# Kernel tuning notes

Hardware: AMD Instinct MI355X
Metric: run time of the kernel (lower is better)

## Reference

```python
import jax, jax.numpy as jnp
import numpy as np

# Dimensions (see shape_source): k=4 -> hk=cobj_size=2
K_LEVEL = 4
HK = K_LEVEL // 2            # conv kernel/stride, == cobj_size
BS = 16                      # MBS*ncobj groups
NUM_TOP = 512
BAG = 50                     # bag size B (orig_fea.shape[1])
D = 512                      # feature dim
H = 512                      # relation-unit hidden dim


def setup_inputs() -> dict:
    key = jax.random.key(0)
    ks = jax.random.split(key, 7)
    orig_fea = jax.random.normal(ks[0], (BS * 2 * HK, BAG, D), jnp.float32)
    ind0 = jax.random.randint(ks[1], (BS, NUM_TOP, HK), 0, BAG, jnp.int32)
    ind1 = jax.random.randint(ks[2], (BS, NUM_TOP, HK), 0, BAG, jnp.int32)
    W0 = jax.random.normal(ks[3], (D, H), jnp.float32) * 0.05
    W1 = jax.random.normal(ks[4], (D, H), jnp.float32) * 0.05
    b = jax.random.normal(ks[5], (H,), jnp.float32) * 0.05
    v = jax.random.normal(ks[6], (H,), jnp.float32) * 0.05
    return {"orig_fea": orig_fea, "ind0": ind0, "ind1": ind1,
            "W0": W0, "W1": W1, "b": b, "v": v}


def reference(orig_fea, ind0, ind1, W0, W1, b, v):
    bs = ind0.shape[0]
    bag = orig_fea.shape[1]
    cobj = ind0.shape[-1]                 # == k//2 == conv kernel hk
    d = orig_fea.shape[-1]

    # create_ids: offset by bag * position so ids index into the flattened half
    offs = (bag * jnp.arange(cobj)).astype(ind0.dtype)
    ids0 = (ind0 + offs).reshape(bs, -1)  # [bs, S], S = num_top*cobj
    ids1 = (ind1 + offs).reshape(bs, -1)

    # rsolo_fea: [bs, 2, X, D] with X = bag*cobj
    fea = orig_fea.reshape(bs, 2, -1, d)

    # relation unit over ALL X*X candidate pairs (dedupe+gather-back in the
    # original is pure memoization; compute-then-gather is the same math)
    h0 = jnp.einsum('bxd,dh->bxh', fea[:, 0], W0)   # [bs, X, H]
    h1 = jnp.einsum('byd,dh->byh', fea[:, 1], W1)   # [bs, X, H]
    hid = jax.nn.relu(h0[:, :, None, :] + h1[:, None, :, :] + b)  # [bs, X, X, H]
    full = jnp.einsum('bxyh,h->bxy', hid, v)        # [bs, X, X]

    # gather rows by ids0, cols by ids1 (per group)
    scores = jax.vmap(lambda f, i0, i1: f[i0][:, i1])(full, ids0, ids1)  # [bs, S, S]

    # Conv2D(1, kernel=hk, stride=hk, ones kernel, zero bias) == block sum-pool
    S = scores.shape[1]
    hk = cobj
    pooled = scores.reshape(bs, S // hk, hk, S // hk, hk).sum(axis=(2, 4))  # [bs, nt, nt]
    out_scores = pooled.reshape(bs, -1, 1)          # [bs, nt*nt, 1]

    nt0, nt1 = ind0.shape[1], ind1.shape[1]
    gi, gj = jnp.meshgrid(jnp.arange(nt0, dtype=jnp.int32),
                          jnp.arange(nt1, dtype=jnp.int32), indexing='ij')
    pairs = jnp.broadcast_to(jnp.stack([gi, gj], axis=-1)[None],
                             (bs, nt0, nt1, 2)).reshape(bs, nt0 * nt1, 2)
    return out_scores, pairs
```

## Files before the change

kernel.cpp:

```cpp
#include <hip/hip_runtime.h>

#define XDIM  100
#define DDIM  512
#define HDIM  512
#define NT    512
#define WS_WT2   0
#define WS_FEA16 1048576
#define WS_V16   4325376
#define WS_H16   4326400
#define WS_FP    7603200

typedef _Float16 h16x8 __attribute__((ext_vector_type(8)));
typedef _Float16 h2    __attribute__((ext_vector_type(2)));
typedef float floatx4  __attribute__((ext_vector_type(4)));

union H8U { h16x8 v; h2 p[4]; unsigned u[4]; };

__global__ void __launch_bounds__(256) prep_k(const float* __restrict__ W0,
                                              const float* __restrict__ W1,
                                              const float* __restrict__ fea,
                                              const float* __restrict__ v,
                                              _Float16* __restrict__ Wt2,
                                              _Float16* __restrict__ fea16,
                                              _Float16* __restrict__ v16) {
    int blk = blockIdx.x;
    int t = threadIdx.x;
    if (blk < 2048) {
        int o  = blk * 256 + t;
        int w  = o >> 18;
        int kb = (o >> 14) & 15;
        int c  = (o >> 5) & 511;
        int qj = o & 31;
        int d  = kb * 32 + qj;
        const float* W = w ? W1 : W0;
        Wt2[o] = (_Float16)W[d * 512 + c];
    } else if (blk < 3648) {
        int tid = (blk - 2048) * 256 + t;
        float4 x = *(const float4*)(fea + (size_t)tid * 4);
        _Float16 r[4] = {(_Float16)x.x, (_Float16)x.y, (_Float16)x.z, (_Float16)x.w};
        *(uint2*)(fea16 + (size_t)tid * 4) = *(const uint2*)r;
    } else {
        v16[t * 2]     = (_Float16)v[t * 2];
        v16[t * 2 + 1] = (_Float16)v[t * 2 + 1];
    }
}

__global__ void __launch_bounds__(256) gemm_k(const _Float16* __restrict__ fea16,
                                              const _Float16* __restrict__ Wt2,
                                              const float* __restrict__ bias,
                                              _Float16* __restrict__ h16) {
    int bx   = blockIdx.x;
    int hb   = bx / 14;
    int rem  = bx % 14;
    int rt   = rem >> 1;
    int chal = rem & 1;
    int w    = threadIdx.x >> 6;
    int lane = threadIdx.x & 63;
    int n0   = (chal * 4 + w) * 64;
    int m0   = rt * 16;
    int s    = hb & 1;
    int l15  = lane & 15;
    int q    = lane >> 4;
    int m    = min(m0 + l15, XDIM - 1);

    const _Float16* ap = fea16 + (size_t)hb * (XDIM * DDIM) + (size_t)m * DDIM + q * 8;
    const _Float16* bp = Wt2 + (size_t)s * 262144 + (size_t)(n0 + l15) * 32 + q * 8;

    floatx4 acc0 = {0.f, 0.f, 0.f, 0.f};
    floatx4 acc1 = acc0, acc2 = acc0, acc3 = acc0;

    for (int kb = 0; kb < 16; ++kb) {
        h16x8 a = *(const h16x8*)(ap + kb * 32);
        const _Float16* bkb = bp + kb * 16384;
        h16x8 b0 = *(const h16x8*)(bkb);
        h16x8 b1 = *(const h16x8*)(bkb + 512);
        h16x8 b2 = *(const h16x8*)(bkb + 1024);
        h16x8 b3 = *(const h16x8*)(bkb + 1536);
        acc0 = __builtin_amdgcn_mfma_f32_16x16x32_f16(a, b0, acc0, 0, 0, 0);
        acc1 = __builtin_amdgcn_mfma_f32_16x16x32_f16(a, b1, acc1, 0, 0, 0);
        acc2 = __builtin_amdgcn_mfma_f32_16x16x32_f16(a, b2, acc2, 0, 0, 0);
        acc3 = __builtin_amdgcn_mfma_f32_16x16x32_f16(a, b3, acc3, 0, 0, 0);
    }

    _Float16* hob = h16 + (size_t)hb * (XDIM * HDIM);
    #pragma unroll
    for (int j = 0; j < 4; ++j) {
        floatx4 a = (j == 0) ? acc0 : (j == 1) ? acc1 : (j == 2) ? acc2 : acc3;
        int col = n0 + 16 * j + l15;
        float bi = s ? bias[col] : 0.f;
        #pragma unroll
        for (int r = 0; r < 4; ++r) {
            int mr = m0 + q * 4 + r;
            if (mr < XDIM) hob[(size_t)mr * HDIM + col] = (_Float16)(a[r] + bi);
        }
    }
}

__global__ void __launch_bounds__(256) full_k(const _Float16* __restrict__ h16,
                                              const _Float16* __restrict__ v16,
                                              float* __restrict__ fp,
                                              float2* __restrict__ pout) {
    int bx  = blockIdx.x;
    int ks  = bx >> 6;
    int rem = bx & 63;
    int b   = rem >> 2;
    int xt  = (rem >> 1) & 1;
    int yt  = rem & 1;
    int x0  = xt * 36;
    int y0  = yt * 36;
    int kc  = ks * 64;

    __shared__ _Float16 sh0[64][72];
    __shared__ unsigned sh1p[32][64];
    __shared__ unsigned sv[32];

    int t = threadIdx.x;
    int r = t & 63, kseg = t >> 6;

    const _Float16* g0 = h16 + ((size_t)(b * 2) * XDIM + x0 + r) * HDIM + kc + kseg * 16;
    *(h16x8*)&sh0[r][kseg * 16]     = *(const h16x8*)g0;
    *(h16x8*)&sh0[r][kseg * 16 + 8] = *(const h16x8*)(g0 + 8);

    const _Float16* g1 = h16 + ((size_t)(b * 2 + 1) * XDIM + y0 + r) * HDIM + kc + kseg * 16;
    H8U u0, u1;
    u0.v = *(const h16x8*)g1;
    u1.v = *(const h16x8*)(g1 + 8);
    #pragma unroll
    for (int pp = 0; pp < 4; ++pp) {
        sh1p[kseg * 8 + pp][r]     = u0.u[pp];
        sh1p[kseg * 8 + 4 + pp][r] = u1.u[pp];
    }
    if (t < 32) sv[t] = *(const unsigned*)(v16 + kc + t * 2);
    __syncthreads();

    {
        size_t pbase = (size_t)bx * 8192;
        #pragma unroll 4
        for (int i = 0; i < 32; ++i) {
            unsigned idx = (unsigned)(pbase + i * 256 + t);
            float2 pr;
            pr.x = (float)((idx >> 9) & 511);
            pr.y = (float)(idx & 511);
            pout[idx] = pr;
        }
    }

    int ty = t >> 4, tx = t & 15;
    float acc[4][4] = {};
    h2 hz; hz[0] = (_Float16)0; hz[1] = (_Float16)0;

    for (int kk = 0; kk < 8; ++kk) {
        H8U a[4];
        #pragma unroll
        for (int i = 0; i < 4; ++i)
            a[i].v = *(const h16x8*)&sh0[ty * 4 + i][kk * 8];
        uint4 bq[4];
        #pragma unroll
        for (int p = 0; p < 4; ++p)
            bq[p] = *(const uint4*)&sh1p[kk * 4 + p][tx * 4];
        uint4 vq = *(const uint4*)&sv[kk * 4];
        const unsigned* vqa = (const unsigned*)&vq;

        #pragma unroll
        for (int p = 0; p < 4; ++p) {
            h2 vp = __builtin_bit_cast(h2, vqa[p]);
            const unsigned* bqa = (const unsigned*)&bq[p];
            #pragma unroll
            for (int i = 0; i < 4; ++i) {
                h2 av = a[i].p[p];
                #pragma unroll
                for (int j = 0; j < 4; ++j) {
                    h2 s = av + __builtin_bit_cast(h2, bqa[j]);
                    s = __builtin_elementwise_max(s, hz);
#if __has_builtin(__builtin_amdgcn_fdot2)
                    acc[i][j] = __builtin_amdgcn_fdot2(s, vp, acc[i][j], false);
#else
                    acc[i][j] += (float)s[0] * (float)vp[0] + (float)s[1] * (float)vp[1];
#endif
                }
            }
        }
    }

    float* fpb = fp + (size_t)(ks * 16 + b) * (XDIM * XDIM);
    #pragma unroll
    for (int i = 0; i < 4; ++i) {
        float4 o;
        o.x = acc[i][0]; o.y = acc[i][1]; o.z = acc[i][2]; o.w = acc[i][3];
        *(float4*)&fpb[(size_t)(x0 + ty * 4 + i) * XDIM + y0 + tx * 4] = o;
    }
}

__global__ void __launch_bounds__(256) score_k(const float* __restrict__ fp,
                                               const int* __restrict__ ind0,
                                               const int* __restrict__ ind1,
                                               float* __restrict__ out) {
    int bx  = blockIdx.x;
    int b   = bx >> 5;
    int rem = bx & 31;
    int it  = rem >> 1;
    int jh  = rem & 1;
    int i0  = it * 32;

    __shared__ float rowsum[32][100];
    __shared__ int a0s[32], a1s[32];
    __shared__ int c0s[256], c1s[256];

    int t = threadIdx.x;
    if (t < 32) {
        int2 ii = *(const int2*)(ind0 + ((size_t)b * NT + i0 + t) * 2);
        a0s[t] = ii.x;
        a1s[t] = ii.y + 50;
    }
    {
        int2 jj = *(const int2*)(ind1 + ((size_t)b * NT + jh * 256 + t) * 2);
        c0s[t] = jj.x;
        c1s[t] = jj.y + 50;
    }
    __syncthreads();

    const float* fb = fp + (size_t)b * (XDIM * XDIM);
    for (int idx = t; idx < 1024; idx += 256) {
        int il = idx >> 5, yq = idx & 31;
        if (yq < 25) {
            float4 s = {0.f, 0.f, 0.f, 0.f};
            int a0 = a0s[il] * XDIM + yq * 4;
            int a1 = a1s[il] * XDIM + yq * 4;
            #pragma unroll
            for (int ksb = 0; ksb < 8; ++ksb) {
                const float* pl = fb + (size_t)ksb * (16 * XDIM * XDIM);
                float4 u = *(const float4*)(pl + a0);
                float4 w = *(const float4*)(pl + a1);
                s.x += u.x + w.x; s.y += u.y + w.y;
                s.z += u.z + w.z; s.w += u.w + w.w;
            }
            *(float4*)&rowsum[il][yq * 4] = s;
        }
    }
    __syncthreads();

    float* sout = out + (size_t)b * (NT * NT) + (size_t)i0 * NT + jh * 256;
    for (int o = t; o < 8192; o += 256) {
        int il = o >> 8, jl = o & 255;
        sout[(size_t)il * NT + jl] = rowsum[il][c0s[jl]] + rowsum[il][c1s[jl]];
    }
}

extern "C" void kernel_launch(void* const* d_in, const int* in_sizes, int n_in,
                              void* d_out, int out_size, void* d_ws, size_t ws_size,
                              hipStream_t stream) {
    const float* fea  = (const float*)d_in[0];
    const int*   ind0 = (const int*)d_in[1];
    const int*   ind1 = (const int*)d_in[2];
    const float* W0   = (const float*)d_in[3];
    const float* W1   = (const float*)d_in[4];
    const float* bias = (const float*)d_in[5];
    const float* v    = (const float*)d_in[6];
    float* out = (float*)d_out;
    char*  ws  = (char*)d_ws;

    _Float16* Wt2   = (_Float16*)(ws + WS_WT2);
    _Float16* fea16 = (_Float16*)(ws + WS_FEA16);
    _Float16* v16   = (_Float16*)(ws + WS_V16);
    _Float16* h16   = (_Float16*)(ws + WS_H16);
    float*    fp    = (float*)(ws + WS_FP);
    float2*   pout  = (float2*)(out + (size_t)16 * NT * NT);

    hipLaunchKernelGGL(prep_k,  dim3(3649), dim3(256), 0, stream, W0, W1, fea, v, Wt2, fea16, v16);
    hipLaunchKernelGGL(gemm_k,  dim3(448),  dim3(256), 0, stream, fea16, Wt2, bias, h16);
    hipLaunchKernelGGL(full_k,  dim3(512),  dim3(256), 0, stream, h16, v16, fp, pout);
    hipLaunchKernelGGL(score_k, dim3(512),  dim3(256), 0, stream, fp, ind0, ind1, out);
}
```

Baseline: 122.0 us.

## Fuse fp32-to-fp16 feature conversion into GEMM and double row tile

```diff
diff --git a/kernel.cpp b/kernel.cpp
--- a/kernel.cpp
+++ b/kernel.cpp
@@ -5,10 +5,9 @@
 #define HDIM  512
 #define NT    512
 #define WS_WT2   0
-#define WS_FEA16 1048576
-#define WS_V16   4325376
-#define WS_H16   4326400
-#define WS_FP    7603200
+#define WS_V16   1048576
+#define WS_H16   1049600
+#define WS_FP    4326400
 
 typedef _Float16 h16x8 __attribute__((ext_vector_type(8)));
 typedef _Float16 h2    __attribute__((ext_vector_type(2)));
@@ -18,10 +17,8 @@
 
 __global__ void __launch_bounds__(256) prep_k(const float* __restrict__ W0,
                                               const float* __restrict__ W1,
-                                              const float* __restrict__ fea,
                                               const float* __restrict__ v,
                                               _Float16* __restrict__ Wt2,
-                                              _Float16* __restrict__ fea16,
                                               _Float16* __restrict__ v16) {
     int blk = blockIdx.x;
     int t = threadIdx.x;
@@ -34,64 +31,79 @@
         int d  = kb * 32 + qj;
         const float* W = w ? W1 : W0;
         Wt2[o] = (_Float16)W[d * 512 + c];
-    } else if (blk < 3648) {
-        int tid = (blk - 2048) * 256 + t;
-        float4 x = *(const float4*)(fea + (size_t)tid * 4);
-        _Float16 r[4] = {(_Float16)x.x, (_Float16)x.y, (_Float16)x.z, (_Float16)x.w};
-        *(uint2*)(fea16 + (size_t)tid * 4) = *(const uint2*)r;
     } else {
         v16[t * 2]     = (_Float16)v[t * 2];
         v16[t * 2 + 1] = (_Float16)v[t * 2 + 1];
     }
 }
 
-__global__ void __launch_bounds__(256) gemm_k(const _Float16* __restrict__ fea16,
+__global__ void __launch_bounds__(256) gemm_k(const float* __restrict__ fea,
                                               const _Float16* __restrict__ Wt2,
                                               const float* __restrict__ bias,
                                               _Float16* __restrict__ h16) {
     int bx   = blockIdx.x;
-    int hb   = bx / 14;
-    int rem  = bx % 14;
-    int rt   = rem >> 1;
-    int chal = rem & 1;
+    int hb   = bx >> 3;
+    int rt   = (bx >> 1) & 3;
+    int chal = bx & 1;
     int w    = threadIdx.x >> 6;
     int lane = threadIdx.x & 63;
     int n0   = (chal * 4 + w) * 64;
-    int m0   = rt * 16;
+    int m0   = rt * 32;
     int s    = hb & 1;
     int l15  = lane & 15;
     int q    = lane >> 4;
-    int m    = min(m0 + l15, XDIM - 1);
-
-    const _Float16* ap = fea16 + (size_t)hb * (XDIM * DDIM) + (size_t)m * DDIM + q * 8;
+    int mA   = min(m0 + l15,      XDIM - 1);
+    int mB   = min(m0 + 16 + l15, XDIM - 1);
+
+    const float* apA = fea + ((size_t)hb * XDIM + mA) * DDIM + q * 8;
+    const float* apB = fea + ((size_t)hb * XDIM + mB) * DDIM + q * 8;
     const _Float16* bp = Wt2 + (size_t)s * 262144 + (size_t)(n0 + l15) * 32 + q * 8;
 
-    floatx4 acc0 = {0.f, 0.f, 0.f, 0.f};
-    floatx4 acc1 = acc0, acc2 = acc0, acc3 = acc0;
+    floatx4 acc[8] = {};
 
     for (int kb = 0; kb < 16; ++kb) {
-        h16x8 a = *(const h16x8*)(ap + kb * 32);
+        float4 a0 = *(const float4*)(apA + kb * 32);
+        float4 a1 = *(const float4*)(apA + kb * 32 + 4);
+        float4 c0 = *(const float4*)(apB + kb * 32);
+        float4 c1 = *(const float4*)(apB + kb * 32 + 4);
+        h16x8 aA, aB;
+        aA[0] = (_Float16)a0.x; aA[1] = (_Float16)a0.y;
+        aA[2] = (_Float16)a0.z; aA[3] = (_Float16)a0.w;
+        aA[4] = (_Float16)a1.x; aA[5] = (_Float16)a1.y;
+        aA[6] = (_Float16)a1.z; aA[7] = (_Float16)a1.w;
+        aB[0] = (_Float16)c0.x; aB[1] = (_Float16)c0.y;
+        aB[2] = (_Float16)c0.z; aB[3] = (_Float16)c0.w;
+        aB[4] = (_Float16)c1.x; aB[5] = (_Float16)c1.y;
+        aB[6] = (_Float16)c1.z; aB[7] = (_Float16)c1.w;
+
         const _Float16* bkb = bp + kb * 16384;
         h16x8 b0 = *(const h16x8*)(bkb);
         h16x8 b1 = *(const h16x8*)(bkb + 512);
         h16x8 b2 = *(const h16x8*)(bkb + 1024);
         h16x8 b3 = *(const h16x8*)(bkb + 1536);
-        acc0 = __builtin_amdgcn_mfma_f32_16x16x32_f16(a, b0, acc0, 0, 0, 0);
-        acc1 = __builtin_amdgcn_mfma_f32_16x16x32_f16(a, b1, acc1, 0, 0, 0);
-        acc2 = __builtin_amdgcn_mfma_f32_16x16x32_f16(a, b2, acc2, 0, 0, 0);
-        acc3 = __builtin_amdgcn_mfma_f32_16x16x32_f16(a, b3, acc3, 0, 0, 0);
+        acc[0] = __builtin_amdgcn_mfma_f32_16x16x32_f16(aA, b0, acc[0], 0, 0, 0);
+        acc[4] = __builtin_amdgcn_mfma_f32_16x16x32_f16(aB, b0, acc[4], 0, 0, 0);
+        acc[1] = __builtin_amdgcn_mfma_f32_16x16x32_f16(aA, b1, acc[1], 0, 0, 0);
+        acc[5] = __builtin_amdgcn_mfma_f32_16x16x32_f16(aB, b1, acc[5], 0, 0, 0);
+        acc[2] = __builtin_amdgcn_mfma_f32_16x16x32_f16(aA, b2, acc[2], 0, 0, 0);
+        acc[6] = __builtin_amdgcn_mfma_f32_16x16x32_f16(aB, b2, acc[6], 0, 0, 0);
+        acc[3] = __builtin_amdgcn_mfma_f32_16x16x32_f16(aA, b3, acc[3], 0, 0, 0);
+        acc[7] = __builtin_amdgcn_mfma_f32_16x16x32_f16(aB, b3, acc[7], 0, 0, 0);
     }
 
     _Float16* hob = h16 + (size_t)hb * (XDIM * HDIM);
     #pragma unroll
-    for (int j = 0; j < 4; ++j) {
-        floatx4 a = (j == 0) ? acc0 : (j == 1) ? acc1 : (j == 2) ? acc2 : acc3;
-        int col = n0 + 16 * j + l15;
-        float bi = s ? bias[col] : 0.f;
-        #pragma unroll
-        for (int r = 0; r < 4; ++r) {
-            int mr = m0 + q * 4 + r;
-            if (mr < XDIM) hob[(size_t)mr * HDIM + col] = (_Float16)(a[r] + bi);
+    for (int mt = 0; mt < 2; ++mt) {
+        #pragma unroll
+        for (int j = 0; j < 4; ++j) {
+            floatx4 a = acc[mt * 4 + j];
+            int col = n0 + 16 * j + l15;
+            float bi = s ? bias[col] : 0.f;
+            #pragma unroll
+            for (int r = 0; r < 4; ++r) {
+                int mr = m0 + mt * 16 + q * 4 + r;
+                if (mr < XDIM) hob[(size_t)mr * HDIM + col] = (_Float16)(a[r] + bi);
+            }
         }
     }
 }
@@ -259,15 +271,14 @@
     float* out = (float*)d_out;
     char*  ws  = (char*)d_ws;
 
-    _Float16* Wt2   = (_Float16*)(ws + WS_WT2);
-    _Float16* fea16 = (_Float16*)(ws + WS_FEA16);
-    _Float16* v16   = (_Float16*)(ws + WS_V16);
-    _Float16* h16   = (_Float16*)(ws + WS_H16);
-    float*    fp    = (float*)(ws + WS_FP);
-    float2*   pout  = (float2*)(out + (size_t)16 * NT * NT);
-
-    hipLaunchKernelGGL(prep_k,  dim3(3649), dim3(256), 0, stream, W0, W1, fea, v, Wt2, fea16, v16);
-    hipLaunchKernelGGL(gemm_k,  dim3(448),  dim3(256), 0, stream, fea16, Wt2, bias, h16);
+    _Float16* Wt2 = (_Float16*)(ws + WS_WT2);
+    _Float16* v16 = (_Float16*)(ws + WS_V16);
+    _Float16* h16 = (_Float16*)(ws + WS_H16);
+    float*    fp  = (float*)(ws + WS_FP);
+    float2*   pout = (float2*)(out + (size_t)16 * NT * NT);
+
+    hipLaunchKernelGGL(prep_k,  dim3(2049), dim3(256), 0, stream, W0, W1, v, Wt2, v16);
+    hipLaunchKernelGGL(gemm_k,  dim3(256),  dim3(256), 0, stream, fea, Wt2, bias, h16);
     hipLaunchKernelGGL(full_k,  dim3(512),  dim3(256), 0, stream, h16, v16, fp, pout);
     hipLaunchKernelGGL(score_k, dim3(512),  dim3(256), 0, stream, fp, ind0, ind1, out);
 }
```

Result: no change. 122.7 us (+0.5%).
